# Performance work log

Hardware: AMD Instinct MI355X
Metric: run time of the kernel (lower is better)

Reference implementation:

```python
import jax, jax.numpy as jnp
import numpy as np

GRID_SIZE = 8
IN_DIM = 1024
OUT_DIM = 1024
BATCH = 4096


def setup_inputs() -> dict:
    key = jax.random.key(0)
    k1, k2, k3 = jax.random.split(key, 3)
    noise_scale = 0.1
    noise_scale_base = 0.1
    x = jax.random.normal(k1, (BATCH, IN_DIM), dtype=jnp.float32)
    scale_base = (1.0 / np.sqrt(IN_DIM)
                  + (jax.random.normal(k2, (OUT_DIM, IN_DIM), dtype=jnp.float32) * 2 - 1)
                  * noise_scale_base)
    scale_spline = jnp.full((OUT_DIM, IN_DIM), 1.0, dtype=jnp.float32)
    coeff = (jax.random.uniform(k3, (2, OUT_DIM, IN_DIM, GRID_SIZE), dtype=jnp.float32)
             * noise_scale / (np.sqrt(IN_DIM) * np.sqrt(GRID_SIZE)))
    return {"x": x, "scale_base": scale_base, "scale_spline": scale_spline,
            "coeff": coeff}


def reference(x, scale_base, scale_spline, coeff):
    # x: (B, I); scale_base/scale_spline: (O, I); coeff: (2, O, I, G)
    G = coeff.shape[-1]
    k = jnp.arange(1, G + 1, dtype=x.dtype)          # (G,)
    ang = x[:, :, None] * k                           # (B, I, G)
    cos_b = jnp.cos(ang)
    sin_b = jnp.sin(ang)
    # fold scale_spline into coeff: (2, O, I, G)
    w = scale_spline[None, :, :, None] * coeff
    spline = (jnp.einsum('big,oig->bo', cos_b, w[0])
              + jnp.einsum('big,oig->bo', sin_b, w[1]))  # (B, O)
    base = jnp.einsum('bi,oi->bo', jax.nn.silu(x), scale_base)
    return base + spline
```

## Files before the change

### kernel.cpp

```cpp
#include <hip/hip_runtime.h>
#include <hip/hip_bf16.h>
#include <stdint.h>

#define BATCH   4096
#define IN_DIM  1024
#define OUT_DIM 1024
#define GRID_G  8
#define K8      16384
#define KB      1024
#define SPLITK  2
#define TPITCH  8192
#define WSCALE  256.0f

typedef __bf16 bf16x8 __attribute__((ext_vector_type(8)));
typedef __bf16 bf16x4 __attribute__((ext_vector_type(4)));
typedef float  f32x4  __attribute__((ext_vector_type(4)));
typedef int    i32x2  __attribute__((ext_vector_type(2)));
typedef int    i32x4  __attribute__((ext_vector_type(4)));
typedef int    i32x8  __attribute__((ext_vector_type(8)));


__global__ __launch_bounds__(256) void prep(const float* __restrict__ x,
                                            const float* __restrict__ sb,
                                            const float* __restrict__ ss,
                                            const float* __restrict__ coeff,
                                            uint8_t* __restrict__ T,
                                            uint8_t* __restrict__ W8,
                                            __bf16* __restrict__ Ab,
                                            __bf16* __restrict__ Wb,
                                            float* __restrict__ C) {
    const int tid = threadIdx.x;

    if (blockIdx.x < 1024) {
        const int t  = blockIdx.x * 256 + tid;
        const int b  = t >> 6;
        const int i0 = (t & 63) * 16;

        {
            float4 z = make_float4(0.f, 0.f, 0.f, 0.f);
            float4* cz = (float4*)(C + (size_t)blockIdx.x * 4096);
#pragma unroll
            for (int j = 0; j < 4; ++j) cz[j * 256 + tid] = z;
        }

        float xv[16];
        {
            const f32x4* xp = (const f32x4*)(x + (size_t)b * IN_DIM + i0);
            f32x4 q0 = __builtin_nontemporal_load(xp + 0);
            f32x4 q1 = __builtin_nontemporal_load(xp + 1);
            f32x4 q2 = __builtin_nontemporal_load(xp + 2);
            f32x4 q3 = __builtin_nontemporal_load(xp + 3);
#pragma unroll
            for (int j = 0; j < 4; ++j) {
                xv[j] = q0[j]; xv[4+j] = q1[j]; xv[8+j] = q2[j]; xv[12+j] = q3[j];
            }
        }

        float c1[16], s1[16];
        bf16x8 va, vb;
#pragma unroll
        for (int j = 0; j < 16; ++j) {
            float e  = __expf(-xv[j]);
            float sl = xv[j] * __builtin_amdgcn_rcpf(1.f + e);
            if (j < 8) va[j & 7] = (__bf16)sl; else vb[j & 7] = (__bf16)sl;
            s1[j] = __sinf(xv[j]);
            c1[j] = __cosf(xv[j]);
        }
        __builtin_nontemporal_store(va, (bf16x8*)(Ab + (size_t)b * IN_DIM + i0));
        __builtin_nontemporal_store(vb, (bf16x8*)(Ab + (size_t)b * IN_DIM + i0 + 8));

        uint8_t* tp = T + (size_t)b * TPITCH + (size_t)i0 * 8;
#pragma unroll
        for (int e2 = 0; e2 < 8; ++e2) {
            f32x4 tv; tv[0] = c1[2*e2]; tv[1] = s1[2*e2]; tv[2] = c1[2*e2+1]; tv[3] = s1[2*e2+1];
            __builtin_nontemporal_store(tv, (f32x4*)(tp + e2 * 16));
        }
    } else {
        const int u = (blockIdx.x - 1024) * 256 + tid;
        const int o = u >> 10;
        const int i = u & 1023;
        const size_t oi = (size_t)o * IN_DIM + i;

        const float s = __builtin_nontemporal_load(ss + oi) * WSCALE;
        {
            float bv = __builtin_nontemporal_load(sb + oi);
            Wb[oi] = (__bf16)bv;
        }
        uint8_t* w8 = W8 + (size_t)o * K8 + (size_t)i * 8;
#pragma unroll
        for (int p = 0; p < 2; ++p) {
            const f32x4* cp = (const f32x4*)(coeff + (((size_t)p * OUT_DIM + o) * IN_DIM + i) * GRID_G);
            f32x4 a0 = __builtin_nontemporal_load(cp + 0);
            f32x4 a1 = __builtin_nontemporal_load(cp + 1);
            int d0 = 0, d1 = 0;
            d0 = __builtin_amdgcn_cvt_pk_fp8_f32(s*a0[0], s*a0[1], d0, false);
            d0 = __builtin_amdgcn_cvt_pk_fp8_f32(s*a0[2], s*a0[3], d0, true);
            d1 = __builtin_amdgcn_cvt_pk_fp8_f32(s*a1[0], s*a1[1], d1, false);
            d1 = __builtin_amdgcn_cvt_pk_fp8_f32(s*a1[2], s*a1[3], d1, true);
            i32x2 dd; dd[0] = d0; dd[1] = d1;
            __builtin_nontemporal_store(dd, (i32x2*)(w8 + (size_t)p * 8192));
        }
    }
}

__global__ __launch_bounds__(256, 2) void gemm_all(const uint8_t* __restrict__ Tg_,
                                                   const uint8_t* __restrict__ W8,
                                                   const uint8_t* __restrict__ Ab,
                                                   const uint8_t* __restrict__ Wb,
                                                   float* __restrict__ C) {
    __shared__ __align__(16) uint8_t pool[81920];
    uint8_t* Abuf  = pool;
    uint8_t* Bb0   = pool + 16384;
    uint8_t* Bb1   = pool + 32768;
    uint8_t* Tb0   = pool + 49152;
    uint8_t* Tb1   = pool + 65536;

    const int tid = threadIdx.x;
    const int w   = tid >> 6;
    const int l   = tid & 63;
    const int flat = blockIdx.y * 8 + blockIdx.x;
    const int xcd  = flat & 7;
    const int idx  = flat >> 3;
    const int bn   = (xcd & 1) * 4 + (idx & 3);
    const int bm   = (xcd >> 1) * 8 + (idx >> 2);
    const int kz  = blockIdx.z;
    const int wm  = w & 1;
    const int wn  = w >> 1;

    f32x4 acc[4][4] = {};

    const int srow   = l >> 3;
    const int schunk = ((l & 7) ^ srow) * 16;
    const int lm = l & 15;
    const int q  = l >> 4;
    const int c0 = (q * 2) << 4, c1 = (q * 2 + 1) << 4;

    {
        const uint8_t* Tg = Tg_ + (size_t)(bm * 128 + w * 32 + srow) * TPITCH + schunk;
        const uint8_t* Bg = W8 + (size_t)(bn * 128 + w * 32 + srow) * K8 + kz * 8192 + schunk;

        auto stageT = [&](uint8_t* dst) {
#pragma unroll
            for (int j = 0; j < 4; ++j)
                __builtin_amdgcn_global_load_lds(
                    (const uint32_t*)(Tg + (size_t)(j * 8) * TPITCH),
                    (uint32_t*)(dst + (w * 32 + j * 8) * 128), 16, 0, 0);
            Tg += 128;
        };
        auto stageB = [&](uint8_t* dst) {
#pragma unroll
            for (int j = 0; j < 4; ++j)
                __builtin_amdgcn_global_load_lds(
                    (const uint32_t*)(Bg + (size_t)(j * 8) * K8),
                    (uint32_t*)(dst + (w * 32 + j * 8) * 128), 16, 0, 0);
            Bg += 128;
        };

        const int r   = tid >> 1;
        const int i8  = tid & 1;
        const int key = r & 7;
        auto agen = [&](const uint8_t* tsrc) {
            const uint8_t* trow = tsrc + r * 128;
            uint8_t*       arow = Abuf + r * 128;
#pragma unroll
            for (int c = 0; c < 4; ++c) {
                const int ch = ((i8 * 4 + c) ^ key) << 4;
                f32x4 tv = *(const f32x4*)(trow + ch);
                i32x4 wv;
#pragma unroll
                for (int e = 0; e < 2; ++e) {
                    float cc = tv[e * 2], sn = tv[e * 2 + 1];
                    float tc = cc + cc;
                    float g1, g2;
                    if (kz == 0) { g1 = cc; g2 = tc * cc - 1.0f; }
                    else         { g1 = sn; g2 = tc * sn; }
                    float g3 = tc * g2 - g1;
                    float g4 = tc * g3 - g2;
                    float g5 = tc * g4 - g3;
                    float g6 = tc * g5 - g4;
                    float g7 = tc * g6 - g5;
                    float g8 = tc * g7 - g6;
                    int d0 = 0, d1 = 0;
                    d0 = __builtin_amdgcn_cvt_pk_fp8_f32(g1, g2, d0, false);
                    d0 = __builtin_amdgcn_cvt_pk_fp8_f32(g3, g4, d0, true);
                    d1 = __builtin_amdgcn_cvt_pk_fp8_f32(g5, g6, d1, false);
                    d1 = __builtin_amdgcn_cvt_pk_fp8_f32(g7, g8, d1, true);
                    wv[e * 2] = d0; wv[e * 2 + 1] = d1;
                }
                *(i32x4*)(arow + ch) = wv;
            }
        };

        auto mfma = [&](const uint8_t* bsrc) {
            i32x8 bf[4];
#pragma unroll
            for (int j = 0; j < 4; ++j) {
                const int row = wn * 64 + j * 16 + lm;
                const int sw  = (row & 7) << 4;
                const uint8_t* rp = bsrc + row * 128;
                i32x4 lo = *(const i32x4*)(rp + (c0 ^ sw));
                i32x4 hi = *(const i32x4*)(rp + (c1 ^ sw));
                bf[j] = __builtin_shufflevector(lo, hi, 0, 1, 2, 3, 4, 5, 6, 7);
            }
#pragma unroll
            for (int i = 0; i < 4; ++i) {
                const int row = wm * 64 + i * 16 + lm;
                const int sw  = (row & 7) << 4;
                const uint8_t* rp = Abuf + row * 128;
                i32x4 lo = *(const i32x4*)(rp + (c0 ^ sw));
                i32x4 hi = *(const i32x4*)(rp + (c1 ^ sw));
                i32x8 af = __builtin_shufflevector(lo, hi, 0, 1, 2, 3, 4, 5, 6, 7);
#pragma unroll
                for (int j = 0; j < 4; ++j)
                    acc[i][j] = __builtin_amdgcn_mfma_scale_f32_16x16x128_f8f6f4(
                        af, bf[j], acc[i][j], 0, 0, 0, 0x7f7f7f7f, 0, 0x7f7f7f7f);
            }
        };

        stageT(Tb0); stageB(Bb0);
        asm volatile("s_waitcnt vmcnt(0)" ::: "memory");
        __builtin_amdgcn_sched_barrier(0);
        __builtin_amdgcn_s_barrier();

        for (int t = 0; t < 64; ++t) {
            const int par = t & 1;
            agen(par ? Tb1 : Tb0);
            if (t < 63) { stageT(par ? Tb0 : Tb1); stageB(par ? Bb0 : Bb1); }
            asm volatile("s_waitcnt lgkmcnt(0)" ::: "memory");
            __builtin_amdgcn_sched_barrier(0);
            if (t < 63) { asm volatile("s_waitcnt vmcnt(8)" ::: "memory"); }
            else        { asm volatile("s_waitcnt vmcnt(0)" ::: "memory"); }
            __builtin_amdgcn_sched_barrier(0);
            __builtin_amdgcn_s_barrier();
            mfma(par ? Bb1 : Bb0);
            if (t < 63) {
                asm volatile("s_waitcnt vmcnt(4)" ::: "memory");
                __builtin_amdgcn_sched_barrier(0);
                __builtin_amdgcn_s_barrier();
            }
        }
    }

#pragma unroll
    for (int i = 0; i < 4; ++i)
#pragma unroll
        for (int j = 0; j < 4; ++j)
            acc[i][j] *= (1.0f / WSCALE);

    __syncthreads();

    {
        uint8_t* A0 = pool;
        uint8_t* A1 = pool + 16384;
        uint8_t* B0 = pool + 32768;
        uint8_t* B1 = pool + 49152;
        const uint8_t* Ag = Ab + (size_t)(bm * 128 + w * 32 + srow) * (KB * 2) + kz * (KB * 2 / SPLITK) + schunk;
        const uint8_t* Bg = Wb + (size_t)(bn * 128 + w * 32 + srow) * (KB * 2) + kz * (KB * 2 / SPLITK) + schunk;

        auto stage = [&](uint8_t* Ad, uint8_t* Bd) {
#pragma unroll
            for (int j = 0; j < 4; ++j) {
                __builtin_amdgcn_global_load_lds(
                    (const uint32_t*)(Ag + (size_t)(j * 8) * (KB * 2)),
                    (uint32_t*)(Ad + (w * 32 + j * 8) * 128), 16, 0, 0);
                __builtin_amdgcn_global_load_lds(
                    (const uint32_t*)(Bg + (size_t)(j * 8) * (KB * 2)),
                    (uint32_t*)(Bd + (w * 32 + j * 8) * 128), 16, 0, 0);
            }
            Ag += 128; Bg += 128;
        };
        auto compute = [&](const uint8_t* Asrc, const uint8_t* Bsrc) {
#pragma unroll
            for (int h = 0; h < 2; ++h) {
                bf16x8 af[4], bfr[4];
#pragma unroll
                for (int i = 0; i < 4; ++i) {
                    const int row = wm * 64 + i * 16 + lm;
                    af[i] = *(const bf16x8*)(Asrc + row * 128 + ((((h * 4 + q) ^ (row & 7))) << 4));
                }
#pragma unroll
                for (int j = 0; j < 4; ++j) {
                    const int row = wn * 64 + j * 16 + lm;
                    bfr[j] = *(const bf16x8*)(Bsrc + row * 128 + ((((h * 4 + q) ^ (row & 7))) << 4));
                }
#pragma unroll
                for (int i = 0; i < 4; ++i)
#pragma unroll
                    for (int j = 0; j < 4; ++j)
                        acc[i][j] = __builtin_amdgcn_mfma_f32_16x16x32_bf16(af[i], bfr[j], acc[i][j], 0, 0, 0);
            }
        };

        stage(A0, B0);
        stage(A1, B1);
        const int NT = (KB * 2 / SPLITK) / 128;
        for (int t = 0; t < NT; ++t) {
            const int par = t & 1;
            if (t < NT - 1) { asm volatile("s_waitcnt vmcnt(8)" ::: "memory"); }
            else            { asm volatile("s_waitcnt vmcnt(0)" ::: "memory"); }
            __builtin_amdgcn_sched_barrier(0);
            __builtin_amdgcn_s_barrier();
            compute(par ? A1 : A0, par ? B1 : B0);
            __builtin_amdgcn_s_barrier();
            if (t < NT - 2) stage(par ? A1 : A0, par ? B1 : B0);
        }
    }

    const int row0 = bm * 128 + wm * 64 + q * 4;
    const int col0 = bn * 128 + wn * 64 + lm;
#pragma unroll
    for (int i = 0; i < 4; ++i)
#pragma unroll
        for (int j = 0; j < 4; ++j)
#pragma unroll
            for (int r = 0; r < 4; ++r)
                unsafeAtomicAdd(&C[(size_t)(row0 + i * 16 + r) * OUT_DIM + col0 + j * 16],
                                acc[i][j][r]);
}

extern "C" void kernel_launch(void* const* d_in, const int* in_sizes, int n_in,
                              void* d_out, int out_size, void* d_ws, size_t ws_size,
                              hipStream_t stream) {
    const float* x     = (const float*)d_in[0];
    const float* sb    = (const float*)d_in[1];
    const float* ss    = (const float*)d_in[2];
    const float* coeff = (const float*)d_in[3];
    float* out = (float*)d_out;

    uint8_t* T  = (uint8_t*)d_ws;
    uint8_t* W8 = T + (size_t)BATCH * TPITCH;
    __bf16*  Ab = (__bf16*)(W8 + (size_t)OUT_DIM * K8);
    __bf16*  Wb = Ab + (size_t)BATCH * KB;

    hipLaunchKernelGGL(prep, dim3(1024 + 4096), dim3(256), 0, stream,
                       x, sb, ss, coeff, T, W8, Ab, Wb, out);
    hipLaunchKernelGGL(gemm_all, dim3(OUT_DIM / 128, BATCH / 128, SPLITK), dim3(256), 0, stream,
                       T, W8, (const uint8_t*)Ab, (const uint8_t*)Wb, out);
}
```

Baseline: 282.3 us.

## Interleave cos/sin features per K chunk, split K four ways, drop double buffering

Reorders the fp8 weight layout so each input index carries its 8 cos and 8 sin coefficients together. The GEMM then builds both cos and sin features via angle-addition recurrence and splits K into four chunks instead of splitting by cos/sin. Shared memory halves and launch bounds allow four blocks per CU, trading the double-buffered async pipeline for simple synchronous stage/sync/compute loops. More split-K chunks mean more atomic adds to the output, and the lost overlap of loads with compute may hurt.

```diff
diff --git a/kernel.cpp b/kernel.cpp
--- a/kernel.cpp
+++ b/kernel.cpp
@@ -8,14 +8,12 @@
 #define GRID_G  8
 #define K8      16384
 #define KB      1024
-#define SPLITK  2
+#define NCHUNK  4
 #define TPITCH  8192
 #define WSCALE  256.0f
 
 typedef __bf16 bf16x8 __attribute__((ext_vector_type(8)));
-typedef __bf16 bf16x4 __attribute__((ext_vector_type(4)));
 typedef float  f32x4  __attribute__((ext_vector_type(4)));
-typedef int    i32x2  __attribute__((ext_vector_type(2)));
 typedef int    i32x4  __attribute__((ext_vector_type(4)));
 typedef int    i32x8  __attribute__((ext_vector_type(8)));
 
@@ -82,38 +80,37 @@
         const size_t oi = (size_t)o * IN_DIM + i;
 
         const float s = __builtin_nontemporal_load(ss + oi) * WSCALE;
-        {
-            float bv = __builtin_nontemporal_load(sb + oi);
-            Wb[oi] = (__bf16)bv;
-        }
-        uint8_t* w8 = W8 + (size_t)o * K8 + (size_t)i * 8;
-#pragma unroll
-        for (int p = 0; p < 2; ++p) {
-            const f32x4* cp = (const f32x4*)(coeff + (((size_t)p * OUT_DIM + o) * IN_DIM + i) * GRID_G);
-            f32x4 a0 = __builtin_nontemporal_load(cp + 0);
-            f32x4 a1 = __builtin_nontemporal_load(cp + 1);
-            int d0 = 0, d1 = 0;
-            d0 = __builtin_amdgcn_cvt_pk_fp8_f32(s*a0[0], s*a0[1], d0, false);
-            d0 = __builtin_amdgcn_cvt_pk_fp8_f32(s*a0[2], s*a0[3], d0, true);
-            d1 = __builtin_amdgcn_cvt_pk_fp8_f32(s*a1[0], s*a1[1], d1, false);
-            d1 = __builtin_amdgcn_cvt_pk_fp8_f32(s*a1[2], s*a1[3], d1, true);
-            i32x2 dd; dd[0] = d0; dd[1] = d1;
-            __builtin_nontemporal_store(dd, (i32x2*)(w8 + (size_t)p * 8192));
-        }
+        Wb[oi] = (__bf16)__builtin_nontemporal_load(sb + oi);
+
+        const f32x4* cp0 = (const f32x4*)(coeff + ((size_t)o * IN_DIM + i) * GRID_G);
+        const f32x4* cp1 = (const f32x4*)(coeff + (((size_t)OUT_DIM + o) * IN_DIM + i) * GRID_G);
+        f32x4 a0 = __builtin_nontemporal_load(cp0 + 0);
+        f32x4 a1 = __builtin_nontemporal_load(cp0 + 1);
+        f32x4 b0 = __builtin_nontemporal_load(cp1 + 0);
+        f32x4 b1 = __builtin_nontemporal_load(cp1 + 1);
+        int w0 = 0, w1 = 0, w2 = 0, w3 = 0;
+        w0 = __builtin_amdgcn_cvt_pk_fp8_f32(s*a0[0], s*a0[1], w0, false);
+        w0 = __builtin_amdgcn_cvt_pk_fp8_f32(s*a0[2], s*a0[3], w0, true);
+        w1 = __builtin_amdgcn_cvt_pk_fp8_f32(s*a1[0], s*a1[1], w1, false);
+        w1 = __builtin_amdgcn_cvt_pk_fp8_f32(s*a1[2], s*a1[3], w1, true);
+        w2 = __builtin_amdgcn_cvt_pk_fp8_f32(s*b0[0], s*b0[1], w2, false);
+        w2 = __builtin_amdgcn_cvt_pk_fp8_f32(s*b0[2], s*b0[3], w2, true);
+        w3 = __builtin_amdgcn_cvt_pk_fp8_f32(s*b1[0], s*b1[1], w3, false);
+        w3 = __builtin_amdgcn_cvt_pk_fp8_f32(s*b1[2], s*b1[3], w3, true);
+        i32x4 out; out[0] = w0; out[1] = w1; out[2] = w2; out[3] = w3;
+        __builtin_nontemporal_store(out, (i32x4*)(W8 + (size_t)o * K8 + (size_t)i * 16));
     }
 }
 
-__global__ __launch_bounds__(256, 2) void gemm_all(const uint8_t* __restrict__ Tg_,
+__global__ __launch_bounds__(256, 4) void gemm_all(const uint8_t* __restrict__ Tg_,
                                                    const uint8_t* __restrict__ W8,
                                                    const uint8_t* __restrict__ Ab,
                                                    const uint8_t* __restrict__ Wb,
                                                    float* __restrict__ C) {
-    __shared__ __align__(16) uint8_t pool[81920];
-    uint8_t* Abuf  = pool;
-    uint8_t* Bb0   = pool + 16384;
-    uint8_t* Bb1   = pool + 32768;
-    uint8_t* Tb0   = pool + 49152;
-    uint8_t* Tb1   = pool + 65536;
+    __shared__ __align__(16) uint8_t pool[40960];
+    uint8_t* Tb = pool;
+    uint8_t* Bb = pool + 8192;
+    uint8_t* Ax = pool + 24576;
 
     const int tid = threadIdx.x;
     const int w   = tid >> 6;
@@ -136,68 +133,76 @@
     const int c0 = (q * 2) << 4, c1 = (q * 2 + 1) << 4;
 
     {
-        const uint8_t* Tg = Tg_ + (size_t)(bm * 128 + w * 32 + srow) * TPITCH + schunk;
-        const uint8_t* Bg = W8 + (size_t)(bn * 128 + w * 32 + srow) * K8 + kz * 8192 + schunk;
-
-        auto stageT = [&](uint8_t* dst) {
-#pragma unroll
-            for (int j = 0; j < 4; ++j)
+        const int trow_l = l >> 2;
+        const int tkey_l = trow_l & 3;
+        const uint8_t* Tg = Tg_ + (size_t)(bm * 128 + w * 32 + trow_l) * TPITCH
+                          + kz * 2048 + (size_t)(((l & 3) ^ tkey_l) * 16);
+        const uint8_t* Bg = W8 + (size_t)(bn * 128 + w * 32 + srow) * K8
+                          + kz * 4096 + schunk;
+
+        auto stageT = [&]() {
+#pragma unroll
+            for (int j = 0; j < 2; ++j)
                 __builtin_amdgcn_global_load_lds(
-                    (const uint32_t*)(Tg + (size_t)(j * 8) * TPITCH),
-                    (uint32_t*)(dst + (w * 32 + j * 8) * 128), 16, 0, 0);
-            Tg += 128;
+                    (const uint32_t*)(Tg + (size_t)(j * 16) * TPITCH),
+                    (uint32_t*)(Tb + w * 2048 + j * 1024), 16, 0, 0);
+            Tg += 64;
         };
-        auto stageB = [&](uint8_t* dst) {
+        auto stageB = [&]() {
 #pragma unroll
             for (int j = 0; j < 4; ++j)
                 __builtin_amdgcn_global_load_lds(
                     (const uint32_t*)(Bg + (size_t)(j * 8) * K8),
-                    (uint32_t*)(dst + (w * 32 + j * 8) * 128), 16, 0, 0);
+                    (uint32_t*)(Bb + (w * 32 + j * 8) * 128), 16, 0, 0);
             Bg += 128;
         };
 
-        const int r   = tid >> 1;
-        const int i8  = tid & 1;
-        const int key = r & 7;
-        auto agen = [&](const uint8_t* tsrc) {
-            const uint8_t* trow = tsrc + r * 128;
-            uint8_t*       arow = Abuf + r * 128;
-#pragma unroll
-            for (int c = 0; c < 4; ++c) {
-                const int ch = ((i8 * 4 + c) ^ key) << 4;
-                f32x4 tv = *(const f32x4*)(trow + ch);
-                i32x4 wv;
+        const int r    = tid >> 1;
+        const int half = tid & 1;
+        const int tkey = r & 3;
+        const int akey = r & 7;
+        const uint8_t* trow = Tb + r * 64;
+        uint8_t*       arow = Ax + r * 128;
+        auto agen = [&]() {
+#pragma unroll
+            for (int c = 0; c < 2; ++c) {
+                f32x4 tv = *(const f32x4*)(trow + (((half * 2 + c) ^ tkey) << 4));
 #pragma unroll
                 for (int e = 0; e < 2; ++e) {
-                    float cc = tv[e * 2], sn = tv[e * 2 + 1];
-                    float tc = cc + cc;
-                    float g1, g2;
-                    if (kz == 0) { g1 = cc; g2 = tc * cc - 1.0f; }
-                    else         { g1 = sn; g2 = tc * sn; }
-                    float g3 = tc * g2 - g1;
-                    float g4 = tc * g3 - g2;
-                    float g5 = tc * g4 - g3;
-                    float g6 = tc * g5 - g4;
-                    float g7 = tc * g6 - g5;
-                    float g8 = tc * g7 - g6;
-                    int d0 = 0, d1 = 0;
-                    d0 = __builtin_amdgcn_cvt_pk_fp8_f32(g1, g2, d0, false);
-                    d0 = __builtin_amdgcn_cvt_pk_fp8_f32(g3, g4, d0, true);
-                    d1 = __builtin_amdgcn_cvt_pk_fp8_f32(g5, g6, d1, false);
-                    d1 = __builtin_amdgcn_cvt_pk_fp8_f32(g7, g8, d1, true);
-                    wv[e * 2] = d0; wv[e * 2 + 1] = d1;
+                    const float cc1 = tv[e * 2], ss1 = tv[e * 2 + 1];
+                    float cg = cc1, sg = ss1;
+                    int w0 = 0, w1 = 0, w2 = 0, w3 = 0;
+                    float cA[8], sA[8];
+                    cA[0] = cg; sA[0] = sg;
+#pragma unroll
+                    for (int g = 1; g < 8; ++g) {
+                        float cn = cg * cc1 - sg * ss1;
+                        float sn = sg * cc1 + cg * ss1;
+                        cg = cn; sg = sn;
+                        cA[g] = cg; sA[g] = sg;
+                    }
+                    w0 = __builtin_amdgcn_cvt_pk_fp8_f32(cA[0], cA[1], w0, false);
+                    w0 = __builtin_amdgcn_cvt_pk_fp8_f32(cA[2], cA[3], w0, true);
+                    w1 = __builtin_amdgcn_cvt_pk_fp8_f32(cA[4], cA[5], w1, false);
+                    w1 = __builtin_amdgcn_cvt_pk_fp8_f32(cA[6], cA[7], w1, true);
+                    w2 = __builtin_amdgcn_cvt_pk_fp8_f32(sA[0], sA[1], w2, false);
+                    w2 = __builtin_amdgcn_cvt_pk_fp8_f32(sA[2], sA[3], w2, true);
+                    w3 = __builtin_amdgcn_cvt_pk_fp8_f32(sA[4], sA[5], w3, false);
+                    w3 = __builtin_amdgcn_cvt_pk_fp8_f32(sA[6], sA[7], w3, true);
+                    i32x4 out; out[0] = w0; out[1] = w1; out[2] = w2; out[3] = w3;
+                    const int ich = half * 4 + c * 2 + e;
+                    *(i32x4*)(arow + ((ich ^ akey) << 4)) = out;
                 }
-                *(i32x4*)(arow + ch) = wv;
             }
         };
 
-        auto mfma = [&](const uint8_t* bsrc) {
+        auto mfma = [&]() {
             i32x8 bf[4];
 #pragma unroll
             for (int j = 0; j < 4; ++j) {
                 const int row = wn * 64 + j * 16 + lm;
                 const int sw  = (row & 7) << 4;
-                const uint8_t* rp = bsrc + row * 128;
+                const uint8_t* rp = Bb + row * 128;
                 i32x4 lo = *(const i32x4*)(rp + (c0 ^ sw));
                 i32x4 hi = *(const i32x4*)(rp + (c1 ^ sw));
                 bf[j] = __builtin_shufflevector(lo, hi, 0, 1, 2, 3, 4, 5, 6, 7);
@@ -206,7 +211,7 @@
             for (int i = 0; i < 4; ++i) {
                 const int row = wm * 64 + i * 16 + lm;
                 const int sw  = (row & 7) << 4;
-                const uint8_t* rp = Abuf + row * 128;
+                const uint8_t* rp = Ax + row * 128;
                 i32x4 lo = *(const i32x4*)(rp + (c0 ^ sw));
                 i32x4 hi = *(const i32x4*)(rp + (c1 ^ sw));
                 i32x8 af = __builtin_shufflevector(lo, hi, 0, 1, 2, 3, 4, 5, 6, 7);
@@ -217,27 +222,13 @@
             }
         };
 
-        stageT(Tb0); stageB(Bb0);
-        asm volatile("s_waitcnt vmcnt(0)" ::: "memory");
-        __builtin_amdgcn_sched_barrier(0);
-        __builtin_amdgcn_s_barrier();
-
-        for (int t = 0; t < 64; ++t) {
-            const int par = t & 1;
-            agen(par ? Tb1 : Tb0);
-            if (t < 63) { stageT(par ? Tb0 : Tb1); stageB(par ? Bb0 : Bb1); }
-            asm volatile("s_waitcnt lgkmcnt(0)" ::: "memory");
-            __builtin_amdgcn_sched_barrier(0);
-            if (t < 63) { asm volatile("s_waitcnt vmcnt(8)" ::: "memory"); }
-            else        { asm volatile("s_waitcnt vmcnt(0)" ::: "memory"); }
-            __builtin_amdgcn_sched_barrier(0);
-            __builtin_amdgcn_s_barrier();
-            mfma(par ? Bb1 : Bb0);
-            if (t < 63) {
-                asm volatile("s_waitcnt vmcnt(4)" ::: "memory");
-                __builtin_amdgcn_sched_barrier(0);
-                __builtin_amdgcn_s_barrier();
-            }
+        for (int t = 0; t < 32; ++t) {
+            stageT(); stageB();
+            __syncthreads();
+            agen();
+            __syncthreads();
+            mfma();
+            __syncthreads();
         }
     }
 
@@ -247,41 +238,37 @@
         for (int j = 0; j < 4; ++j)
             acc[i][j] *= (1.0f / WSCALE);
 
-    __syncthreads();
-
     {
-        uint8_t* A0 = pool;
-        uint8_t* A1 = pool + 16384;
-        uint8_t* B0 = pool + 32768;
-        uint8_t* B1 = pool + 49152;
-        const uint8_t* Ag = Ab + (size_t)(bm * 128 + w * 32 + srow) * (KB * 2) + kz * (KB * 2 / SPLITK) + schunk;
-        const uint8_t* Bg = Wb + (size_t)(bn * 128 + w * 32 + srow) * (KB * 2) + kz * (KB * 2 / SPLITK) + schunk;
-
-        auto stage = [&](uint8_t* Ad, uint8_t* Bd) {
+        uint8_t* As = pool;
+        uint8_t* Bs = pool + 16384;
+        const uint8_t* Ag = Ab + (size_t)(bm * 128 + w * 32 + srow) * (KB * 2) + kz * 512 + schunk;
+        const uint8_t* Bg = Wb + (size_t)(bn * 128 + w * 32 + srow) * (KB * 2) + kz * 512 + schunk;
+
+        for (int t = 0; t < 4; ++t) {
 #pragma unroll
             for (int j = 0; j < 4; ++j) {
                 __builtin_amdgcn_global_load_lds(
                     (const uint32_t*)(Ag + (size_t)(j * 8) * (KB * 2)),
-                    (uint32_t*)(Ad + (w * 32 + j * 8) * 128), 16, 0, 0);
+                    (uint32_t*)(As + (w * 32 + j * 8) * 128), 16, 0, 0);
                 __builtin_amdgcn_global_load_lds(
                     (const uint32_t*)(Bg + (size_t)(j * 8) * (KB * 2)),
-                    (uint32_t*)(Bd + (w * 32 + j * 8) * 128), 16, 0, 0);
+                    (uint32_t*)(Bs + (w * 32 + j * 8) * 128), 16, 0, 0);
             }
             Ag += 128; Bg += 128;
-        };
-        auto compute = [&](const uint8_t* Asrc, const uint8_t* Bsrc) {
+            __syncthreads();
+
 #pragma unroll
             for (int h = 0; h < 2; ++h) {
                 bf16x8 af[4], bfr[4];
 #pragma unroll
                 for (int i = 0; i < 4; ++i) {
                     const int row = wm * 64 + i * 16 + lm;
-                    af[i] = *(const bf16x8*)(Asrc + row * 128 + ((((h * 4 + q) ^ (row & 7))) << 4));
+                    af[i] = *(const bf16x8*)(As + row * 128 + ((((h * 4 + q) ^ (row & 7))) << 4));
                 }
 #pragma unroll
                 for (int j = 0; j < 4; ++j) {
                     const int row = wn * 64 + j * 16 + lm;
-                    bfr[j] = *(const bf16x8*)(Bsrc + row * 128 + ((((h * 4 + q) ^ (row & 7))) << 4));
+                    bfr[j] = *(const bf16x8*)(Bs + row * 128 + ((((h * 4 + q) ^ (row & 7))) << 4));
                 }
 #pragma unroll
                 for (int i = 0; i < 4; ++i)
@@ -289,20 +276,7 @@
                     for (int j = 0; j < 4; ++j)
                         acc[i][j] = __builtin_amdgcn_mfma_f32_16x16x32_bf16(af[i], bfr[j], acc[i][j], 0, 0, 0);
             }
-        };
-
-        stage(A0, B0);
-        stage(A1, B1);
-        const int NT = (KB * 2 / SPLITK) / 128;
-        for (int t = 0; t < NT; ++t) {
-            const int par = t & 1;
-            if (t < NT - 1) { asm volatile("s_waitcnt vmcnt(8)" ::: "memory"); }
-            else            { asm volatile("s_waitcnt vmcnt(0)" ::: "memory"); }
-            __builtin_amdgcn_sched_barrier(0);
-            __builtin_amdgcn_s_barrier();
-            compute(par ? A1 : A0, par ? B1 : B0);
-            __builtin_amdgcn_s_barrier();
-            if (t < NT - 2) stage(par ? A1 : A0, par ? B1 : B0);
+            __syncthreads();
         }
     }
 
@@ -334,6 +308,6 @@
 
     hipLaunchKernelGGL(prep, dim3(1024 + 4096), dim3(256), 0, stream,
                        x, sb, ss, coeff, T, W8, Ab, Wb, out);
-    hipLaunchKernelGGL(gemm_all, dim3(OUT_DIM / 128, BATCH / 128, SPLITK), dim3(256), 0, stream,
+    hipLaunchKernelGGL(gemm_all, dim3(OUT_DIM / 128, BATCH / 128, NCHUNK), dim3(256), 0, stream,
                        T, W8, (const uint8_t*)Ab, (const uint8_t*)Wb, out);
 }
```

Measured after the change: 307.1 us. 8.8% more time.
